# Optimization experiments

Hardware: AMD Instinct MI355X
Metric: run time of the kernel (lower is better)

The kernel has to match this reference:

```python
import jax, jax.numpy as jnp
import numpy as np

STRIDES = (8, 16, 32, 64, 128)
NUM_CONVS = 4
GROUPS = 32
EPS = 1e-5
FEAT_SHAPES = [(8, 256, 100, 152), (8, 256, 50, 76), (8, 256, 25, 38), (8, 256, 13, 19), (8, 256, 7, 10)]


def _conv3x3(x, w, b):
    # x: [B,C,H,W], w: [O,I,3,3] -> SAME padding, stride 1
    y = jax.lax.conv_general_dilated(x, w, (1, 1), 'SAME', dimension_numbers=('NCHW', 'OIHW', 'NCHW'))
    return y + b[None, :, None, None]


def _group_norm(x, g, b):
    B, C, H, W = x.shape
    xr = x.reshape(B, GROUPS, C // GROUPS, H, W)
    m = xr.mean(axis=(2, 3, 4), keepdims=True)
    v = xr.var(axis=(2, 3, 4), keepdims=True)
    xr = (xr - m) * jax.lax.rsqrt(v + EPS)
    return xr.reshape(B, C, H, W) * g[None, :, None, None] + b[None, :, None, None]


def _head(feats, cls_w, cls_b, cls_gn_g, cls_gn_b, box_w, box_b, box_gn_g, box_gn_b,
          logits_w, logits_b, ctr_w, ctr_b, reg_w, reg_b, scales):
    outs = []
    for l, f in enumerate(feats):
        ct, bt = f, f
        for i in range(NUM_CONVS):  # fixed-depth tower loop
            ct = jax.nn.relu(_group_norm(_conv3x3(ct, cls_w[i], cls_b[i]), cls_gn_g[i], cls_gn_b[i]))
            bt = jax.nn.relu(_group_norm(_conv3x3(bt, box_w[i], box_b[i]), box_gn_g[i], box_gn_b[i]))
        logits = _conv3x3(ct, logits_w, logits_b)          # [B,80,H,W]
        ctr = _conv3x3(ct, ctr_w, ctr_b)                   # [B,1,H,W]
        reg = jnp.exp(scales[l] * _conv3x3(bt, reg_w, reg_b))  # [B,4,H,W], torch.exp(Scale(bbox_pred))
        B = f.shape[0]
        outs.append(jnp.concatenate([logits, reg, ctr], axis=1).reshape(B, -1))
    return jnp.concatenate(outs, axis=1)  # [B, sum_l 85*H_l*W_l]


def _locations(feats):
    # FCOS grid locations: (x,y) center of each stride cell, per level, concatenated
    locs = []
    for l, f in enumerate(feats):
        h, w = f.shape[-2:]
        s = STRIDES[l]
        sx = jnp.arange(w, dtype=jnp.float32) * s + s // 2
        sy = jnp.arange(h, dtype=jnp.float32) * s + s // 2
        yy, xx = jnp.meshgrid(sy, sx, indexing='ij')
        locs.append(jnp.stack([xx.reshape(-1), yy.reshape(-1)], axis=1))
    return jnp.concatenate(locs, axis=0)  # [sum HW, 2]


def setup_inputs() -> dict:
    key = jax.random.key(0)
    ks = jax.random.split(key, 12)
    d = {}
    for i, s in enumerate(FEAT_SHAPES):
        d['feat%d' % i] = jax.random.normal(ks[i], s, dtype=jnp.float32)

    def w(k, shape):
        return jax.random.normal(k, shape, dtype=jnp.float32) * 0.01  # init std=0.01

    d['cls_w'] = w(ks[5], (NUM_CONVS, 256, 256, 3, 3))
    d['cls_b'] = jnp.zeros((NUM_CONVS, 256), jnp.float32)
    d['cls_gn_g'] = jnp.ones((NUM_CONVS, 256), jnp.float32)
    d['cls_gn_b'] = jnp.zeros((NUM_CONVS, 256), jnp.float32)
    d['box_w'] = w(ks[6], (NUM_CONVS, 256, 256, 3, 3))
    d['box_b'] = jnp.zeros((NUM_CONVS, 256), jnp.float32)
    d['box_gn_g'] = jnp.ones((NUM_CONVS, 256), jnp.float32)
    d['box_gn_b'] = jnp.zeros((NUM_CONVS, 256), jnp.float32)
    d['logits_w'] = w(ks[7], (80, 256, 3, 3))
    d['logits_b'] = jnp.full((80,), -float(np.log((1.0 - 0.01) / 0.01)), jnp.float32)  # prior_prob bias
    d['ctr_w'] = w(ks[8], (1, 256, 3, 3))
    d['ctr_b'] = jnp.zeros((1,), jnp.float32)
    d['reg_w'] = w(ks[9], (4, 256, 3, 3))
    d['reg_b'] = jnp.zeros((4,), jnp.float32)
    d['scales'] = jnp.ones((5,), jnp.float32)
    return d


def reference(feat0, feat1, feat2, feat3, feat4, cls_w, cls_b, cls_gn_g, cls_gn_b,
              box_w, box_b, box_gn_g, box_gn_b, logits_w, logits_b, ctr_w, ctr_b,
              reg_w, reg_b, scales):
    feats = [feat0, feat1, feat2, feat3, feat4]
    out = _head(feats, cls_w, cls_b, cls_gn_g, cls_gn_b, box_w, box_b, box_gn_g, box_gn_b,
                logits_w, logits_b, ctr_w, ctr_b, reg_w, reg_b, scales)
    locs = _locations(feats)
    return out, locs
```

## Files before the change

### kernel.cpp

```cpp
#include <hip/hip_runtime.h>
#include <hip/hip_bf16.h>

#define TOT85 1722695ULL

using short8 = __attribute__((ext_vector_type(8))) short;
using f32x4  = __attribute__((ext_vector_type(4))) float;

struct Feat5 { const float* p[5]; };
struct TowerPtrs {
  const __hip_bfloat16* wpk;
  const float* bias;
  const float* statsIn;
  const float* gamma;
  const float* beta;
  const __hip_bfloat16* src;
  __hip_bfloat16* dst;
  float* statsOut;
};
struct TowerArgs { TowerPtrs t0, t1; };

__device__ __forceinline__ float bfbits2f(short u) {
  return __uint_as_float(((unsigned int)(unsigned short)u) << 16);
}
__device__ __forceinline__ short f2bfbits(float f) {
  __hip_bfloat16 h = __float2bfloat16(f);
  return *reinterpret_cast<short*>(&h);
}

#define LVL_TABLES                                                              \
  constexpr int kH[5] = {100, 50, 25, 13, 7};                                   \
  constexpr int kW[5] = {152, 76, 38, 19, 10};                                  \
  constexpr int kNTx[5] = {10, 5, 3, 2, 1};                                     \
  constexpr int kCumT[5] = {0, 130, 165, 177, 181};                             \
  constexpr int kCumHW[5] = {0, 15200, 19000, 19950, 20197};                    \
  constexpr float kInv[5] = {1.f / 121600.f, 1.f / 30400.f, 1.f / 7600.f,       \
                             1.f / 1976.f, 1.f / 560.f};

__global__ __launch_bounds__(256) void repack_tower_k(const float* __restrict__ cls_w,
                                                      const float* __restrict__ box_w,
                                                      __hip_bfloat16* __restrict__ dst_cls,
                                                      __hip_bfloat16* __restrict__ dst_box) {
  const size_t TW = (size_t)9 * 8 * 256 * 32;
  int y = blockIdx.y;
  const float* src = (y < 4) ? cls_w + (size_t)y * 256 * 2304
                             : box_w + (size_t)(y - 4) * 256 * 2304;
  __hip_bfloat16* dst = (y < 4) ? dst_cls + (size_t)y * TW
                                : dst_box + (size_t)(y - 4) * TW;
  int idx = blockIdx.x * 256 + threadIdx.x;
  int o = idx / 2304;
  int r = idx - o * 2304;
  int i = r / 9;
  int t = r - i * 9;
  dst[((size_t)(t * 8 + (i >> 5)) * 256 + o) * 32 + (i & 31)] =
      __float2bfloat16(src[idx]);
}

__global__ __launch_bounds__(256) void repack_k(const float* __restrict__ src,
                                                __hip_bfloat16* __restrict__ dst,
                                                int O, int NOCP, int ocoff) {
  int idx = blockIdx.x * 256 + threadIdx.x;
  if (idx >= O * 2304) return;
  int o = idx / 2304;
  int r = idx - o * 2304;
  int i = r / 9;
  int t = r - i * 9;
  dst[((size_t)(t * 8 + (i >> 5)) * NOCP + (o + ocoff)) * 32 + (i & 31)] =
      __float2bfloat16(src[idx]);
}

__global__ void locations_all_k(float* __restrict__ out) {
  LVL_TABLES
  constexpr int kStride[5] = {8, 16, 32, 64, 128};
  int i = blockIdx.x * 256 + threadIdx.x;
  if (i >= 20267) return;
  int lvl = (i >= 15200) + (i >= 19000) + (i >= 19950) + (i >= 20197);
  int local = i - kCumHW[lvl];
  int W = kW[lvl];
  float s = (float)kStride[lvl];
  int y = local / W, x = local - y * W;
  out[2 * i + 0] = x * s + 0.5f * s;
  out[2 * i + 1] = y * s + 0.5f * s;
}

template <bool NORM_IN, bool SRC_NCHW>
__global__ __launch_bounds__(256, 2) void conv_tower_k(Feat5 feats, TowerArgs args) {
  LVL_TABLES
  __shared__ __align__(16) short s_in[180 * 72];
  __shared__ float s_red[64];
  __shared__ float s_a[256], s_c[256];

  TowerPtrs P;
  if (blockIdx.y == 0) P = args.t0; else P = args.t1;

  const int tid = threadIdx.x;
  const int lane = tid & 63;
  const int wave = tid >> 6;
  const int wm = wave >> 1;
  const int wn = wave & 1;
  const int bx = blockIdx.x;
  const int lvl = (bx >= 130) + (bx >= 165) + (bx >= 177) + (bx >= 181);
  const int H = kH[lvl], W = kW[lvl], nTx = kNTx[lvl];
  const int tloc = bx - kCumT[lvl];
  const int ty = tloc / nTx, tx = tloc - ty * nTx;
  const int x0 = tx * 16, y0 = ty * 8;
  const int b = blockIdx.z;
  const int HW = H * W;
  const size_t lbase = (size_t)2048 * kCumHW[lvl];
  const int l15 = lane & 15;
  const int kg = lane >> 4;
  const int q8x = (tid & 7) * 8;

  if (tid < 64) s_red[tid] = 0.f;
  if (NORM_IN) {
    const float* statsIn = P.statsIn + (size_t)lvl * 4096;
    float inv_cnt = kInv[lvl];
    int g = tid >> 3;
    float s = statsIn[(b * 32 + g) * 2 + 0];
    float ss = statsIn[(b * 32 + g) * 2 + 1];
    float m = s * inv_cnt;
    float var = fmaf(-m, m, ss * inv_cnt);
    float rs = rsqrtf(var + 1e-5f);
    float avv = rs * P.gamma[tid];
    s_a[tid] = avv;
    s_c[tid] = fmaf(-m, avv, P.beta[tid]);
  }

  f32x4 acc[4][8];
#pragma unroll
  for (int m = 0; m < 4; ++m)
#pragma unroll
    for (int n = 0; n < 8; ++n) acc[m][n] = (f32x4){0.f, 0.f, 0.f, 0.f};

  const short* wlane = (const short*)P.wpk + ((wn * 128 + l15) * 32 + kg * 8);

  const int pixN = tid;
  int prowN = pixN / 18;
  int pcolN = pixN - prowN * 18;
  const int gyN = y0 + prowN - 1, gxN = x0 + pcolN - 1;
  const bool validN = (pixN < 180) && (gyN >= 0 && gyN < H && gxN >= 0 && gxN < W);

  for (int c = 0; c < 4; ++c) {
    const int ic0 = c * 64;

    short8 pv[6];
    float fv[32];
    if (SRC_NCHW) {
      const float* srcf = feats.p[lvl];
      if (validN) {
        const float* p = srcf + (((size_t)(b * 256 + ic0)) * H + gyN) * W + gxN;
#pragma unroll
        for (int j = 0; j < 32; ++j) fv[j] = p[(size_t)j * HW];
      }
    } else {
      const short* srcb = (const short*)P.src + lbase;
#pragma unroll
      for (int r = 0; r < 6; ++r) {
        int idx = r * 256 + tid;
        pv[r] = (short8)0;
        if (idx < 1440) {
          int px = idx >> 3;
          int prow = px / 18;
          int pcol = px - prow * 18;
          int gy = y0 + prow - 1, gx = x0 + pcol - 1;
          if (gy >= 0 && gy < H && gx >= 0 && gx < W)
            pv[r] = *(const short8*)(srcb +
                                     ((((size_t)b * H + gy) * W + gx) * 256 + ic0 + q8x));
        }
      }
    }

    __syncthreads();

    if (SRC_NCHW) {
      const float* srcf = feats.p[lvl];
      if (pixN < 180) {
        short8 sv[4];
        if (validN) {
#pragma unroll
          for (int q = 0; q < 4; ++q)
#pragma unroll
            for (int j = 0; j < 8; ++j) sv[q][j] = f2bfbits(fv[q * 8 + j]);
        } else {
#pragma unroll
          for (int q = 0; q < 4; ++q) sv[q] = (short8)0;
        }
#pragma unroll
        for (int q = 0; q < 4; ++q) *(short8*)(s_in + pixN * 72 + q * 8) = sv[q];
        if (validN) {
          const float* p = srcf + (((size_t)(b * 256 + ic0 + 32)) * H + gyN) * W + gxN;
#pragma unroll
          for (int j = 0; j < 32; ++j) fv[j] = p[(size_t)j * HW];
#pragma unroll
          for (int q = 0; q < 4; ++q)
#pragma unroll
            for (int j = 0; j < 8; ++j) sv[q][j] = f2bfbits(fv[q * 8 + j]);
        }
#pragma unroll
        for (int q = 0; q < 4; ++q) *(short8*)(s_in + pixN * 72 + 32 + q * 8) = sv[q];
      }
    } else {
      float av[8], cv[8];
#pragma unroll
      for (int j = 0; j < 8; ++j) {
        int c2 = ic0 + q8x + j;
        av[j] = s_a[c2];
        cv[j] = s_c[c2];
      }
#pragma unroll
      for (int r = 0; r < 6; ++r) {
        int idx = r * 256 + tid;
        if (idx < 1440) {
          int px = idx >> 3;
          int prow = px / 18;
          int pcol = px - prow * 18;
          int gy = y0 + prow - 1, gx = x0 + pcol - 1;
          short8 o8 = (short8)0;
          if (gy >= 0 && gy < H && gx >= 0 && gx < W) {
#pragma unroll
            for (int j = 0; j < 8; ++j)
              o8[j] = f2bfbits(fmaxf(fmaf(bfbits2f(pv[r][j]), av[j], cv[j]), 0.f));
          }
          *(short8*)(s_in + px * 72 + q8x) = o8;
        }
      }
    }
    __syncthreads();

    const short* wcb = wlane + (size_t)c * 2 * 8192;
    short8 bwA[8], bwB[8];
#pragma unroll
    for (int n = 0; n < 8; ++n) bwA[n] = *(const short8*)(wcb + n * 512);

    auto kbody = [&](int k, short8* curw, short8* nxtw) {
      if (k < 17) {
        int kn = k + 1;
        const short* wt = wcb + ((size_t)((kn >> 1) * 8 + (kn & 1))) * 8192;
#pragma unroll
        for (int n = 0; n < 8; ++n) nxtw[n] = *(const short8*)(wt + n * 512);
      }
      const int tap = k >> 1, sub = k & 1;
      const int dy = tap / 3, dx = tap - dy * 3;
      short8 af[4];
#pragma unroll
      for (int m = 0; m < 4; ++m)
        af[m] = *(const short8*)(s_in + ((wm * 4 + m + dy) * 18 + (l15 + dx)) * 72 +
                                 sub * 32 + kg * 8);
#pragma unroll
      for (int m = 0; m < 4; ++m)
#pragma unroll
        for (int n = 0; n < 8; ++n)
          acc[m][n] = __builtin_amdgcn_mfma_f32_16x16x32_bf16(af[m], curw[n], acc[m][n], 0, 0, 0);
    };
#pragma unroll
    for (int k = 0; k < 18; k += 2) {
      kbody(k, bwA, bwB);
      kbody(k + 1, bwB, bwA);
    }
  }

  short* dst = (short*)P.dst + lbase;
  const int masks[5] = {1, 2, 4, 16, 32};
#pragma unroll
  for (int n = 0; n < 8; ++n) {
    int oc_g = wn * 128 + n * 16 + l15;
    float bv = P.bias[oc_g];
    float lsum = 0.f, lssq = 0.f;
#pragma unroll
    for (int m = 0; m < 4; ++m) {
      int oy = y0 + wm * 4 + m;
#pragma unroll
      for (int r = 0; r < 4; ++r) {
        int ox = x0 + kg * 4 + r;
        bool valid = (oy < H) && (ox < W);
        float v = acc[m][n][r] + bv;
        if (valid) {
          dst[(((size_t)b * H + oy) * W + ox) * 256 + oc_g] = f2bfbits(v);
          lsum += v;
          lssq += v * v;
        }
      }
    }
#pragma unroll
    for (int s = 0; s < 5; ++s) {
      lsum += __shfl_xor(lsum, masks[s], 64);
      lssq += __shfl_xor(lssq, masks[s], 64);
    }
    if ((lane & 55) == 0) {
      int g2 = ((wn * 8 + n) * 2 + ((lane >> 3) & 1)) * 2;
      atomicAdd(&s_red[g2 + 0], lsum);
      atomicAdd(&s_red[g2 + 1], lssq);
    }
  }
  __syncthreads();
  float* statsOut = P.statsOut + (size_t)lvl * 4096;
  if (tid < 64) atomicAdd(&statsOut[(size_t)b * 64 + tid], s_red[tid]);
}

template <int NREP, int OUT_MODE>
__global__ __launch_bounds__(256, 3) void conv_head_k(
    const __hip_bfloat16* __restrict__ srcb_base, const __hip_bfloat16* __restrict__ wpk,
    const float* __restrict__ bias, const float* __restrict__ bias2,
    const float* __restrict__ statsInBase, const float* __restrict__ gamma,
    const float* __restrict__ beta, float* __restrict__ out,
    const float* __restrict__ scales, int NOCP) {
  LVL_TABLES
  __shared__ __align__(16) short s_in[180 * 40];
  __shared__ float s_a[256], s_c[256];

  const int tid = threadIdx.x;
  const int lane = tid & 63;
  const int wave = tid >> 6;
  const int wm = wave >> 1;
  const int wn = wave & 1;
  const int bx = blockIdx.x;
  const int lvl = (bx >= 130) + (bx >= 165) + (bx >= 177) + (bx >= 181);
  const int H = kH[lvl], W = kW[lvl], nTx = kNTx[lvl];
  const int tloc = bx - kCumT[lvl];
  const int ty = tloc / nTx, tx = tloc - ty * nTx;
  const int x0 = tx * 16, y0 = ty * 8;
  const int b = blockIdx.z;
  const int HW = H * W;
  const size_t lbase = (size_t)2048 * kCumHW[lvl];
  float* out_lvl = out + (size_t)85 * kCumHW[lvl];
  const int l15 = lane & 15;
  const int kg = lane >> 4;
  const int q8 = (tid & 3) * 8;

  {
    const float* statsIn = statsInBase + (size_t)lvl * 4096;
    float inv_cnt = kInv[lvl];
    int g = tid >> 3;
    float s = statsIn[(b * 32 + g) * 2 + 0];
    float ss = statsIn[(b * 32 + g) * 2 + 1];
    float m = s * inv_cnt;
    float var = fmaf(-m, m, ss * inv_cnt);
    float rs = rsqrtf(var + 1e-5f);
    float avv = rs * gamma[tid];
    s_a[tid] = avv;
    s_c[tid] = fmaf(-m, avv, beta[tid]);
  }

  f32x4 acc[4][NREP];
#pragma unroll
  for (int m = 0; m < 4; ++m)
#pragma unroll
    for (int n = 0; n < NREP; ++n) acc[m][n] = (f32x4){0.f, 0.f, 0.f, 0.f};

  const short* wlane = (const short*)wpk + ((wn * NREP * 16 + l15) * 32 + kg * 8);
  const size_t TAPSTR = (size_t)8 * NOCP * 32;

  for (int chunk = 0; chunk < 8; ++chunk) {
    const int ic0 = chunk * 32;
    __syncthreads();
    {
      const short* srcb = (const short*)srcb_base + lbase;
      float av[8], cv[8];
#pragma unroll
      for (int j = 0; j < 8; ++j) {
        int c2 = ic0 + q8 + j;
        av[j] = s_a[c2];
        cv[j] = s_c[c2];
      }
      for (int idx = tid; idx < 720; idx += 256) {
        int pix = idx >> 2;
        int prow = pix / 18;
        int pcol = pix - prow * 18;
        int gy = y0 + prow - 1, gx = x0 + pcol - 1;
        short8 o8 = (short8)0;
        if (gy >= 0 && gy < H && gx >= 0 && gx < W) {
          const short* sp = srcb + ((((size_t)b * H + gy) * W + gx) * 256 + ic0 + q8);
          short8 v8 = *(const short8*)sp;
#pragma unroll
          for (int j = 0; j < 8; ++j)
            o8[j] = f2bfbits(fmaxf(fmaf(bfbits2f(v8[j]), av[j], cv[j]), 0.f));
        }
        *(short8*)(s_in + pix * 40 + q8) = o8;
      }
    }
    __syncthreads();

    const short* wch = wlane + (size_t)chunk * NOCP * 32;
    short8 bwA[NREP], bwB[NREP];
#pragma unroll
    for (int n = 0; n < NREP; ++n) bwA[n] = *(const short8*)(wch + n * 512);

    auto tapbody = [&](int tap, short8* curw, short8* nxtw) {
      if (tap < 8) {
        const short* wt = wch + (size_t)(tap + 1) * TAPSTR;
#pragma unroll
        for (int n = 0; n < NREP; ++n) nxtw[n] = *(const short8*)(wt + n * 512);
      }
      const int dy = tap / 3, dx = tap - dy * 3;
      short8 af[4];
#pragma unroll
      for (int m = 0; m < 4; ++m)
        af[m] = *(const short8*)(s_in + ((wm * 4 + m + dy) * 18 + (l15 + dx)) * 40 + kg * 8);
#pragma unroll
      for (int m = 0; m < 4; ++m)
#pragma unroll
        for (int n = 0; n < NREP; ++n)
          acc[m][n] = __builtin_amdgcn_mfma_f32_16x16x32_bf16(af[m], curw[n], acc[m][n], 0, 0, 0);
    };
#pragma unroll
    for (int tap = 0; tap < 9; tap += 2) {
      tapbody(tap, bwA, bwB);
      if (tap + 1 < 9) tapbody(tap + 1, bwB, bwA);
    }
  }

#pragma unroll
  for (int n = 0; n < NREP; ++n) {
    int oc_l = wn * NREP * 16 + n * 16 + l15;
    int oc_valid = (OUT_MODE == 1) ? 81 : 4;
    float bv;
    if (OUT_MODE == 1)
      bv = (oc_l < 80) ? bias[oc_l] : ((oc_l == 80) ? bias2[0] : 0.f);
    else
      bv = (oc_l < oc_valid) ? bias[oc_l] : 0.f;
#pragma unroll
    for (int m = 0; m < 4; ++m) {
      int oy = y0 + wm * 4 + m;
#pragma unroll
      for (int r = 0; r < 4; ++r) {
        int ox = x0 + kg * 4 + r;
        bool valid = (oy < H) && (ox < W) && (oc_l < oc_valid);
        float v = acc[m][n][r] + bv;
        if (valid) {
          if (OUT_MODE == 1) {
            int och = (oc_l == 80) ? 84 : oc_l;
            out_lvl[(size_t)b * TOT85 + (size_t)och * HW + oy * W + ox] = v;
          } else {
            out_lvl[(size_t)b * TOT85 + (size_t)(80 + oc_l) * HW + oy * W + ox] =
                expf(scales[lvl] * v);
          }
        }
      }
    }
  }
}

extern "C" void kernel_launch(void* const* d_in, const int* in_sizes, int n_in,
                              void* d_out_v, int out_size, void* d_ws, size_t ws_size,
                              hipStream_t stream) {
  (void)in_sizes; (void)n_in; (void)out_size;

  Feat5 feats;
  for (int i = 0; i < 5; ++i) feats.p[i] = (const float*)d_in[i];
  const float* cls_w = (const float*)d_in[5];
  const float* cls_b = (const float*)d_in[6];
  const float* cls_g = (const float*)d_in[7];
  const float* cls_bb = (const float*)d_in[8];
  const float* box_w = (const float*)d_in[9];
  const float* box_b = (const float*)d_in[10];
  const float* box_g = (const float*)d_in[11];
  const float* box_bb = (const float*)d_in[12];
  const float* logits_w = (const float*)d_in[13];
  const float* logits_b = (const float*)d_in[14];
  const float* ctr_w = (const float*)d_in[15];
  const float* ctr_b = (const float*)d_in[16];
  const float* reg_w = (const float*)d_in[17];
  const float* reg_b = (const float*)d_in[18];
  const float* scales = (const float*)d_in[19];
  float* d_out = (float*)d_out_v;

  char* wsp = (char*)d_ws;
  size_t off = 0;
  auto carve = [&](size_t bytes) -> char* {
    char* p = wsp + off;
    off += (bytes + 255) & ~(size_t)255;
    return p;
  };
  const size_t ALLE = (size_t)8 * 20267 * 256;
  const size_t ALLEb = ALLE * 2;
  const size_t TW = (size_t)9 * 8 * 256 * 32;
  const size_t FIXED = 8 * TW * 2 + (size_t)9 * 8 * 96 * 32 * 2 +
                       (size_t)9 * 8 * 32 * 32 * 2 + (size_t)40 * 512 * 4 + 64 * 256;
  const bool fused = (ws_size >= 4 * ALLEb + FIXED);

  __hip_bfloat16 *bufCA, *bufCB, *bufBA, *bufBB;
  bufCA = (__hip_bfloat16*)carve(ALLEb);
  bufCB = (__hip_bfloat16*)carve(ALLEb);
  if (fused) {
    bufBA = (__hip_bfloat16*)carve(ALLEb);
    bufBB = (__hip_bfloat16*)carve(ALLEb);
  } else {
    bufBA = bufCA;
    bufBB = bufCB;
  }
  __hip_bfloat16* wpk_cls = (__hip_bfloat16*)carve(4 * TW * 2);
  __hip_bfloat16* wpk_box = (__hip_bfloat16*)carve(4 * TW * 2);
  __hip_bfloat16* wpk_clsh = (__hip_bfloat16*)carve((size_t)9 * 8 * 96 * 32 * 2);
  __hip_bfloat16* wpk_regh = (__hip_bfloat16*)carve((size_t)9 * 8 * 32 * 32 * 2);
  float* stats_all = (float*)carve((size_t)40 * 512 * 4);

  hipMemsetAsync(stats_all, 0, (size_t)40 * 512 * 4, stream);

  hipLaunchKernelGGL(repack_tower_k, dim3(2304, 8), dim3(256), 0, stream, cls_w, box_w,
                     wpk_cls, wpk_box);
  auto rp = [&](const float* s, __hip_bfloat16* d, int O, int NOCP, int ocoff) {
    int total = O * 2304;
    hipLaunchKernelGGL(repack_k, dim3((total + 255) / 256), dim3(256), 0, stream, s, d, O, NOCP,
                       ocoff);
  };
  rp(logits_w, wpk_clsh, 80, 96, 0);
  rp(ctr_w, wpk_clsh, 1, 96, 80);
  rp(reg_w, wpk_regh, 4, 32, 0);

  const size_t OUT0 = (size_t)8 * TOT85;
  hipLaunchKernelGGL(locations_all_k, dim3(80), dim3(256), 0, stream, d_out + OUT0);

  auto slot = [&](int t, int i) { return stats_all + (size_t)(t * 4 + i) * 512; };
  auto mkPtrs = [&](int t, int i, const __hip_bfloat16* src, __hip_bfloat16* dst) {
    TowerPtrs p;
    p.wpk = ((t == 0) ? wpk_cls : wpk_box) + (size_t)i * TW;
    p.bias = ((t == 0) ? cls_b : box_b) + i * 256;
    p.statsIn = (i == 0) ? nullptr : slot(t, i - 1);
    p.gamma = (i == 0) ? nullptr : ((t == 0) ? cls_g : box_g) + (i - 1) * 256;
    p.beta = (i == 0) ? nullptr : ((t == 0) ? cls_bb : box_bb) + (i - 1) * 256;
    p.src = src;
    p.dst = dst;
    p.statsOut = slot(t, i);
    return p;
  };

  dim3 blk(256);
  __hip_bfloat16 *curC = bufCA, *nxtC = bufCB, *curB = bufBA, *nxtB = bufBB;

  if (fused) {
    dim3 gridF(182, 2, 8);
    for (int i = 0; i < 4; ++i) {
      TowerArgs a;
      if (i == 0) {
        a.t0 = mkPtrs(0, 0, nullptr, curC);
        a.t1 = mkPtrs(1, 0, nullptr, curB);
        hipLaunchKernelGGL((conv_tower_k<false, true>), gridF, blk, 0, stream, feats, a);
      } else {
        a.t0 = mkPtrs(0, i, curC, nxtC);
        a.t1 = mkPtrs(1, i, curB, nxtB);
        hipLaunchKernelGGL((conv_tower_k<true, false>), gridF, blk, 0, stream, feats, a);
        __hip_bfloat16* tc = curC; curC = nxtC; nxtC = tc;
        __hip_bfloat16* tb = curB; curB = nxtB; nxtB = tb;
      }
    }
    hipLaunchKernelGGL((conv_head_k<3, 1>), dim3(182, 1, 8), blk, 0, stream,
                       (const __hip_bfloat16*)curC, wpk_clsh, logits_b, ctr_b, slot(0, 3),
                       cls_g + 3 * 256, cls_bb + 3 * 256, d_out, scales, 96);
    hipLaunchKernelGGL((conv_head_k<1, 2>), dim3(182, 1, 8), blk, 0, stream,
                       (const __hip_bfloat16*)curB, wpk_regh, reg_b, (const float*)nullptr,
                       slot(1, 3), box_g + 3 * 256, box_bb + 3 * 256, d_out, scales, 32);
  } else {
    dim3 gridS(182, 1, 8);
    for (int t = 0; t < 2; ++t) {
      __hip_bfloat16* cur = bufCA;
      __hip_bfloat16* nxt = bufCB;
      {
        TowerArgs a;
        a.t0 = mkPtrs(t, 0, nullptr, cur);
        a.t1 = a.t0;
        hipLaunchKernelGGL((conv_tower_k<false, true>), gridS, blk, 0, stream, feats, a);
      }
      for (int i = 1; i < 4; ++i) {
        TowerArgs a;
        a.t0 = mkPtrs(t, i, cur, nxt);
        a.t1 = a.t0;
        hipLaunchKernelGGL((conv_tower_k<true, false>), gridS, blk, 0, stream, feats, a);
        __hip_bfloat16* tmp = cur; cur = nxt; nxt = tmp;
      }
      if (t == 0) {
        hipLaunchKernelGGL((conv_head_k<3, 1>), gridS, blk, 0, stream,
                           (const __hip_bfloat16*)cur, wpk_clsh, logits_b, ctr_b, slot(0, 3),
                           cls_g + 3 * 256, cls_bb + 3 * 256, d_out, scales, 96);
      } else {
        hipLaunchKernelGGL((conv_head_k<1, 2>), gridS, blk, 0, stream,
                           (const __hip_bfloat16*)cur, wpk_regh, reg_b, (const float*)nullptr,
                           slot(1, 3), box_g + 3 * 256, box_bb + 3 * 256, d_out, scales, 32);
      }
    }
  }
}
```

Measured before the change: 2.394 ms.

## Stream tower conv weights into LDS via async global_load_lds double buffering

Tower conv weights are now repacked into a swizzled per-step layout and loaded straight into per-wave LDS double buffers with global_load_lds. Loads for step K+2 overlap the MFMAs of step K, with manual vmcnt waits replacing the register prefetch of weights from global memory. The input channel chunk drops from 64 to 32, halving the input tile in LDS to make room for the 64KB weight buffers. The change adds more barriers per output (8 chunks instead of 4) and hand-written waitcnt ordering that must match the exact instruction count. It also raises LDS use, which may limit the two-blocks-per-CU occupancy target.

```diff
diff --git a/kernel.cpp b/kernel.cpp
--- a/kernel.cpp
+++ b/kernel.cpp
@@ -3,6 +3,7 @@
 
 #define TOT85 1722695ULL
 
+using bfx4   = __attribute__((ext_vector_type(4))) short;
 using short8 = __attribute__((ext_vector_type(8))) short;
 using f32x4  = __attribute__((ext_vector_type(4))) float;
 
@@ -26,6 +27,11 @@
   __hip_bfloat16 h = __float2bfloat16(f);
   return *reinterpret_cast<short*>(&h);
 }
+__device__ __forceinline__ void gload_lds16(const void* g, void* l) {
+  __builtin_amdgcn_global_load_lds(
+      (const __attribute__((address_space(1))) unsigned int*)g,
+      (__attribute__((address_space(3))) unsigned int*)l, 16, 0, 0);
+}
 
 #define LVL_TABLES                                                              \
   constexpr int kH[5] = {100, 50, 25, 13, 7};                                   \
@@ -40,7 +46,7 @@
                                                       const float* __restrict__ box_w,
                                                       __hip_bfloat16* __restrict__ dst_cls,
                                                       __hip_bfloat16* __restrict__ dst_box) {
-  const size_t TW = (size_t)9 * 8 * 256 * 32;
+  const size_t TW = (size_t)72 * 2 * 4096;
   int y = blockIdx.y;
   const float* src = (y < 4) ? cls_w + (size_t)y * 256 * 2304
                              : box_w + (size_t)(y - 4) * 256 * 2304;
@@ -51,8 +57,11 @@
   int r = idx - o * 2304;
   int i = r / 9;
   int t = r - i * 9;
-  dst[((size_t)(t * 8 + (i >> 5)) * 256 + o) * 32 + (i & 31)] =
-      __float2bfloat16(src[idx]);
+  int step = (i >> 5) * 9 + t;
+  int wn = o >> 7, oc = o & 127;
+  int blk = (oc << 2) | ((i >> 3) & 3);
+  int blkS = blk ^ (oc & 7);
+  dst[(((size_t)step * 2 + wn) * 512 + blkS) * 8 + (i & 7)] = __float2bfloat16(src[idx]);
 }
 
 __global__ __launch_bounds__(256) void repack_k(const float* __restrict__ src,
@@ -85,8 +94,8 @@
 template <bool NORM_IN, bool SRC_NCHW>
 __global__ __launch_bounds__(256, 2) void conv_tower_k(Feat5 feats, TowerArgs args) {
   LVL_TABLES
-  __shared__ __align__(16) short s_in[180 * 72];
-  __shared__ float s_red[64];
+  __shared__ __align__(16) short s_in[180 * 36];
+  __shared__ __align__(16) short s_wf[4 * 2 * 4096];
   __shared__ float s_a[256], s_c[256];
 
   TowerPtrs P;
@@ -108,9 +117,8 @@
   const size_t lbase = (size_t)2048 * kCumHW[lvl];
   const int l15 = lane & 15;
   const int kg = lane >> 4;
-  const int q8x = (tid & 7) * 8;
-
-  if (tid < 64) s_red[tid] = 0.f;
+  const int q8 = (tid & 3) * 8;
+
   if (NORM_IN) {
     const float* statsIn = P.statsIn + (size_t)lvl * 4096;
     float inv_cnt = kInv[lvl];
@@ -131,7 +139,16 @@
 #pragma unroll
     for (int n = 0; n < 8; ++n) acc[m][n] = (f32x4){0.f, 0.f, 0.f, 0.f};
 
-  const short* wlane = (const short*)P.wpk + ((wn * 128 + l15) * 32 + kg * 8);
+  const short* wbase = (const short*)P.wpk;
+  short* mybuf = s_wf + wave * 8192;
+  const int wfoff = (((4 * l15 + kg) ^ (l15 & 7))) * 8;
+
+  auto gldsK = [&](int K) {
+    const short* ws = wbase + ((size_t)(K * 2 + wn)) * 4096 + lane * 8;
+    short* db = mybuf + (K & 1) * 4096;
+#pragma unroll
+    for (int r = 0; r < 8; ++r) gload_lds16(ws + r * 512, db + r * 512);
+  };
 
   const int pixN = tid;
   int prowN = pixN / 18;
@@ -139,10 +156,10 @@
   const int gyN = y0 + prowN - 1, gxN = x0 + pcolN - 1;
   const bool validN = (pixN < 180) && (gyN >= 0 && gyN < H && gxN >= 0 && gxN < W);
 
-  for (int c = 0; c < 4; ++c) {
-    const int ic0 = c * 64;
-
-    short8 pv[6];
+  for (int c = 0; c < 8; ++c) {
+    const int ic0 = c * 32;
+
+    short8 pv[3];
     float fv[32];
     if (SRC_NCHW) {
       const float* srcf = feats.p[lvl];
@@ -154,109 +171,119 @@
     } else {
       const short* srcb = (const short*)P.src + lbase;
 #pragma unroll
-      for (int r = 0; r < 6; ++r) {
+      for (int r = 0; r < 3; ++r) {
         int idx = r * 256 + tid;
         pv[r] = (short8)0;
-        if (idx < 1440) {
-          int px = idx >> 3;
+        if (idx < 720) {
+          int px = idx >> 2;
           int prow = px / 18;
           int pcol = px - prow * 18;
           int gy = y0 + prow - 1, gx = x0 + pcol - 1;
           if (gy >= 0 && gy < H && gx >= 0 && gx < W)
             pv[r] = *(const short8*)(srcb +
-                                     ((((size_t)b * H + gy) * W + gx) * 256 + ic0 + q8x));
+                                     ((((size_t)b * H + gy) * W + gx) * 256 + ic0 + q8));
         }
       }
     }
 
-    __syncthreads();
+    asm volatile("s_waitcnt lgkmcnt(0)" ::: "memory");
+    __builtin_amdgcn_s_barrier();
 
     if (SRC_NCHW) {
-      const float* srcf = feats.p[lvl];
       if (pixN < 180) {
-        short8 sv[4];
-        if (validN) {
-#pragma unroll
-          for (int q = 0; q < 4; ++q)
-#pragma unroll
-            for (int j = 0; j < 8; ++j) sv[q][j] = f2bfbits(fv[q * 8 + j]);
-        } else {
-#pragma unroll
-          for (int q = 0; q < 4; ++q) sv[q] = (short8)0;
+#pragma unroll
+        for (int q = 0; q < 4; ++q) {
+          bfx4 lo = (bfx4)0, hi = (bfx4)0;
+          if (validN) {
+#pragma unroll
+            for (int j = 0; j < 4; ++j) {
+              lo[j] = f2bfbits(fv[q * 8 + j]);
+              hi[j] = f2bfbits(fv[q * 8 + 4 + j]);
+            }
+          }
+          *(bfx4*)(s_in + pixN * 36 + q * 8) = lo;
+          *(bfx4*)(s_in + pixN * 36 + q * 8 + 4) = hi;
         }
-#pragma unroll
-        for (int q = 0; q < 4; ++q) *(short8*)(s_in + pixN * 72 + q * 8) = sv[q];
-        if (validN) {
-          const float* p = srcf + (((size_t)(b * 256 + ic0 + 32)) * H + gyN) * W + gxN;
-#pragma unroll
-          for (int j = 0; j < 32; ++j) fv[j] = p[(size_t)j * HW];
-#pragma unroll
-          for (int q = 0; q < 4; ++q)
-#pragma unroll
-            for (int j = 0; j < 8; ++j) sv[q][j] = f2bfbits(fv[q * 8 + j]);
-        }
-#pragma unroll
-        for (int q = 0; q < 4; ++q) *(short8*)(s_in + pixN * 72 + 32 + q * 8) = sv[q];
       }
     } else {
       float av[8], cv[8];
 #pragma unroll
       for (int j = 0; j < 8; ++j) {
-        int c2 = ic0 + q8x + j;
+        int c2 = ic0 + q8 + j;
         av[j] = s_a[c2];
         cv[j] = s_c[c2];
       }
 #pragma unroll
-      for (int r = 0; r < 6; ++r) {
+      for (int r = 0; r < 3; ++r) {
         int idx = r * 256 + tid;
-        if (idx < 1440) {
-          int px = idx >> 3;
-          int prow = px / 18;
-          int pcol = px - prow * 18;
-          int gy = y0 + prow - 1, gx = x0 + pcol - 1;
-          short8 o8 = (short8)0;
-          if (gy >= 0 && gy < H && gx >= 0 && gx < W) {
-#pragma unroll
-            for (int j = 0; j < 8; ++j)
-              o8[j] = f2bfbits(fmaxf(fmaf(bfbits2f(pv[r][j]), av[j], cv[j]), 0.f));
+        if (idx < 720) {
+          int px = idx >> 2;
+          bfx4 lo = (bfx4)0, hi = (bfx4)0;
+          {
+            int prow = px / 18;
+            int pcol = px - prow * 18;
+            int gy = y0 + prow - 1, gx = x0 + pcol - 1;
+            if (gy >= 0 && gy < H && gx >= 0 && gx < W) {
+#pragma unroll
+              for (int j = 0; j < 4; ++j) {
+                lo[j] = f2bfbits(fmaxf(fmaf(bfbits2f(pv[r][j]), av[j], cv[j]), 0.f));
+                hi[j] = f2bfbits(fmaxf(fmaf(bfbits2f(pv[r][j + 4]), av[j + 4], cv[j + 4]), 0.f));
+              }
+            }
           }
-          *(short8*)(s_in + px * 72 + q8x) = o8;
+          *(bfx4*)(s_in + px * 36 + q8) = lo;
+          *(bfx4*)(s_in + px * 36 + q8 + 4) = hi;
         }
       }
     }
-    __syncthreads();
-
-    const short* wcb = wlane + (size_t)c * 2 * 8192;
-    short8 bwA[8], bwB[8];
-#pragma unroll
-    for (int n = 0; n < 8; ++n) bwA[n] = *(const short8*)(wcb + n * 512);
-
-    auto kbody = [&](int k, short8* curw, short8* nxtw) {
-      if (k < 17) {
-        int kn = k + 1;
-        const short* wt = wcb + ((size_t)((kn >> 1) * 8 + (kn & 1))) * 8192;
-#pragma unroll
-        for (int n = 0; n < 8; ++n) nxtw[n] = *(const short8*)(wt + n * 512);
-      }
-      const int tap = k >> 1, sub = k & 1;
+    if (c == 0) { gldsK(0); gldsK(1); }
+
+    asm volatile("s_waitcnt lgkmcnt(0)" ::: "memory");
+    __builtin_amdgcn_s_barrier();
+
+#pragma unroll
+    for (int tap = 0; tap < 9; ++tap) {
+      const int K = c * 9 + tap;
+      const int par = (c & 1) ^ (tap & 1);
+      if (c == 7 && tap == 8)
+        asm volatile("s_waitcnt vmcnt(0)" ::: "memory");
+      else
+        asm volatile("s_waitcnt vmcnt(8)" ::: "memory");
+
       const int dy = tap / 3, dx = tap - dy * 3;
+      short8 wf[8];
+      {
+        const short* wb = mybuf + par * 4096 + wfoff;
+#pragma unroll
+        for (int n = 0; n < 8; ++n) wf[n] = *(const short8*)(wb + n * 512);
+      }
       short8 af[4];
 #pragma unroll
+      for (int m = 0; m < 4; ++m) {
+        const short* ab = s_in + ((wm * 4 + m + dy) * 18 + (l15 + dx)) * 36 + kg * 8;
+        bfx4 lo = *(const bfx4*)(ab);
+        bfx4 hi = *(const bfx4*)(ab + 4);
+        short8 v;
+#pragma unroll
+        for (int j = 0; j < 4; ++j) { v[j] = lo[j]; v[j + 4] = hi[j]; }
+        af[m] = v;
+      }
+      asm volatile("s_waitcnt lgkmcnt(0)" ::: "memory");
+      __builtin_amdgcn_sched_barrier(0);
+      if (K + 2 < 72) gldsK(K + 2);
+
+#pragma unroll
       for (int m = 0; m < 4; ++m)
-        af[m] = *(const short8*)(s_in + ((wm * 4 + m + dy) * 18 + (l15 + dx)) * 72 +
-                                 sub * 32 + kg * 8);
-#pragma unroll
-      for (int m = 0; m < 4; ++m)
 #pragma unroll
         for (int n = 0; n < 8; ++n)
-          acc[m][n] = __builtin_amdgcn_mfma_f32_16x16x32_bf16(af[m], curw[n], acc[m][n], 0, 0, 0);
-    };
-#pragma unroll
-    for (int k = 0; k < 18; k += 2) {
-      kbody(k, bwA, bwB);
-      kbody(k + 1, bwB, bwA);
-    }
-  }
+          acc[m][n] = __builtin_amdgcn_mfma_f32_16x16x32_bf16(af[m], wf[n], acc[m][n], 0, 0, 0);
+    }
+  }
+
+  __syncthreads();
+  float* s_red = (float*)s_wf;
+  if (tid < 64) s_red[tid] = 0.f;
+  __syncthreads();
 
   short* dst = (short*)P.dst + lbase;
   const int masks[5] = {1, 2, 4, 16, 32};
@@ -472,7 +499,7 @@
   };
   const size_t ALLE = (size_t)8 * 20267 * 256;
   const size_t ALLEb = ALLE * 2;
-  const size_t TW = (size_t)9 * 8 * 256 * 32;
+  const size_t TW = (size_t)72 * 2 * 4096;
   const size_t FIXED = 8 * TW * 2 + (size_t)9 * 8 * 96 * 32 * 2 +
                        (size_t)9 * 8 * 32 * 32 * 2 + (size_t)40 * 512 * 4 + 64 * 256;
   const bool fused = (ws_size >= 4 * ALLEb + FIXED);
```

Result: slower. 3.498 ms (+46.1%).
